# Optimization experiments

Hardware: AMD Instinct MI355X
Metric: run time of the kernel (lower is better)

Reference implementation:

```python
import jax, jax.numpy as jnp
import numpy as np

B, L, D, H = 2, 2048, 2048, 16
DH = D // H
SCALE = 1.0 / float(np.sqrt(DH))


def setup_inputs() -> dict:
    key = jax.random.key(0)
    ks = jax.random.split(key, 5)
    std = 1.0 / float(np.sqrt(D))
    return {
        "x": jax.random.normal(ks[0], (B, L, D), dtype=jnp.float32),
        "W_q": jax.random.normal(ks[1], (D, D), dtype=jnp.float32) * std,
        "W_k": jax.random.normal(ks[2], (D, D), dtype=jnp.float32) * std,
        "W_v": jax.random.normal(ks[3], (D, D), dtype=jnp.float32) * std,
        "W_o": jax.random.normal(ks[4], (D, D), dtype=jnp.float32) * std,
    }


def _split_heads(t):
    # (B, L, D) -> (B, H, L, DH)
    b, l, _ = t.shape
    return t.reshape(b, l, H, DH).transpose(0, 2, 1, 3)


def reference(x, W_q, W_k, W_v, W_o):
    # nn.Linear(bias=False): y = x @ W.T
    q = _split_heads(x @ W_q.T)  # (B,H,L,DH)
    k = _split_heads(x @ W_k.T)
    v = _split_heads(x @ W_v.T)
    scores = jnp.einsum("bhqd,bhkd->bhqk", q, k) * SCALE  # (B,H,L,L)
    causal = jnp.arange(L)[:, None] >= jnp.arange(L)[None, :]  # True = keep
    scores = jnp.where(causal[None, None], scores, -jnp.inf)
    attn = jax.nn.softmax(scores, axis=-1)
    y = jnp.einsum("bhqk,bhkd->bhqd", attn, v)  # (B,H,L,DH)
    y = y.transpose(0, 2, 1, 3).reshape(B, L, D)  # merge heads
    return y @ W_o.T
```

## Files before the change

### kernel.cpp

```cpp
#include <hip/hip_runtime.h>
#include <hip/hip_bf16.h>
#include <stdint.h>

typedef unsigned short u16;
typedef __bf16 bf16x8 __attribute__((ext_vector_type(8)));
typedef float f32x4 __attribute__((ext_vector_type(4)));

#define SEQ    2048
#define DMODEL 2048
#define NHEAD  16
#define DHEAD  128
#define QSCALE (0.088388347648318447f * 1.4426950408889634f)

__device__ __forceinline__ u16 f2bf(float f){
  uint32_t u = __float_as_uint(f);
  u += 0x7FFFu + ((u >> 16) & 1u);
  return (u16)(u >> 16);
}

__device__ __forceinline__ void gload_lds16(const u16* g, u16* l){
  __builtin_amdgcn_global_load_lds((const __attribute__((address_space(1))) void*)g,
                                   (__attribute__((address_space(3))) void*)l,
                                   16, 0, 0);
}

__global__ __launch_bounds__(256) void cvt_bf16(const float* __restrict__ src,
                                                u16* __restrict__ dst, int n4){
  int i = blockIdx.x * 256 + threadIdx.x;
  if (i < n4){
    float4 v = reinterpret_cast<const float4*>(src)[i];
    ushort4 o;
    o.x = f2bf(v.x); o.y = f2bf(v.y); o.z = f2bf(v.z); o.w = f2bf(v.w);
    reinterpret_cast<ushort4*>(dst)[i] = o;
  }
}

__global__ __launch_bounds__(256) void cvt_w4(const float* __restrict__ Wq,
    const float* __restrict__ Wk, const float* __restrict__ Wv,
    const float* __restrict__ Wo, u16* __restrict__ dst){
  const int z = blockIdx.y;
  const float* s = (z==0) ? Wq : (z==1) ? Wk : (z==2) ? Wv : Wo;
  int i = blockIdx.x * 256 + threadIdx.x;
  float4 v = reinterpret_cast<const float4*>(s)[i];
  ushort4 o;
  o.x = f2bf(v.x); o.y = f2bf(v.y); o.z = f2bf(v.z); o.w = f2bf(v.w);
  reinterpret_cast<ushort4*>(dst + (size_t)z*4194304)[i] = o;
}

__device__ __forceinline__ void stageA(const u16* __restrict__ G, int grow0, int kt,
                                       int half, u16* lds, int w, int lane){
  #pragma unroll
  for (int j = 0; j < 2; ++j){
    int q   = w*2 + j;
    int r0  = ((q & 8) << 4) + half*64 + (q & 7)*8;
    int row = r0 + (lane >> 3);
    int sc  = (lane & 7) ^ (row & 7);
    gload_lds16(G + (size_t)(grow0 + row)*DMODEL + kt*64 + sc*8, lds + r0*64);
  }
}
__device__ __forceinline__ void stageB(const u16* __restrict__ G, int grow0, int kt,
                                       int half, u16* lds, int w, int lane){
  #pragma unroll
  for (int j = 0; j < 2; ++j){
    int q   = w*2 + j;
    int r0  = ((q >> 2) << 6) + half*32 + (q & 3)*8;
    int row = r0 + (lane >> 3);
    int sc  = (lane & 7) ^ (row & 7);
    gload_lds16(G + (size_t)(grow0 + row)*DMODEL + kt*64 + sc*8, lds + r0*64);
  }
}

__device__ __forceinline__ bf16x8 ldsf(const u16* lds, int row, int c){
  return *reinterpret_cast<const bf16x8*>(lds + row*64 + (((c ^ (row & 7)) & 7) << 3));
}

template<int MH>
__device__ __forceinline__ void load_a(bf16x8 (&a)[4][2], const u16* LA,
                                       int wr, int ln, int g){
  #pragma unroll
  for (int m = 0; m < 4; ++m){
    int row = wr*128 + MH*64 + m*16 + ln;
    a[m][0] = ldsf(LA, row, g);
    a[m][1] = ldsf(LA, row, 4 + g);
  }
}
template<int NH>
__device__ __forceinline__ void load_b(bf16x8 (&b)[2][2], const u16* LB,
                                       int wc, int ln, int g){
  #pragma unroll
  for (int n = 0; n < 2; ++n){
    int row = wc*64 + NH*32 + n*16 + ln;
    b[n][0] = ldsf(LB, row, g);
    b[n][1] = ldsf(LB, row, 4 + g);
  }
}

template<int MH, int NH>
__device__ __forceinline__ void mfma_quad(f32x4 (&acc)[8][4], bf16x8 (&a)[4][2],
                                          bf16x8 (&b)[2][2]){
  __builtin_amdgcn_s_setprio(1);
  #pragma unroll
  for (int m = 0; m < 4; ++m)
    #pragma unroll
    for (int n = 0; n < 2; ++n){
      acc[MH*4+m][NH*2+n] = __builtin_amdgcn_mfma_f32_16x16x32_bf16(
          a[m][0], b[n][0], acc[MH*4+m][NH*2+n], 0, 0, 0);
      acc[MH*4+m][NH*2+n] = __builtin_amdgcn_mfma_f32_16x16x32_bf16(
          a[m][1], b[n][1], acc[MH*4+m][NH*2+n], 0, 0, 0);
    }
  __builtin_amdgcn_s_setprio(0);
}

__device__ __forceinline__ void phase_pre(){
  __builtin_amdgcn_s_barrier();
  asm volatile("s_waitcnt lgkmcnt(0)" ::: "memory");
  __builtin_amdgcn_sched_barrier(0);
}

__device__ __forceinline__ void gemm8_core(const u16* __restrict__ A,
    const u16* __restrict__ W, int bm, int bnl,
    u16 (*ldsA)[256*64], u16 (*ldsB)[256*64], f32x4 (&acc)[8][4],
    int w, int lane, int wr, int wc, int g, int ln){
  const f32x4 z4 = {0.f,0.f,0.f,0.f};
  #pragma unroll
  for (int i = 0; i < 8; ++i)
    #pragma unroll
    for (int j = 0; j < 4; ++j) acc[i][j] = z4;

  stageA(A, bm, 0, 0, ldsA[0], w, lane);
  stageB(W, bnl, 0, 1, ldsB[0], w, lane);
  stageA(A, bm, 0, 1, ldsA[0], w, lane);
  stageB(W, bnl, 0, 0, ldsB[0], w, lane);
  stageA(A, bm, 1, 0, ldsA[1], w, lane);
  stageB(W, bnl, 1, 1, ldsB[1], w, lane);
  asm volatile("s_waitcnt vmcnt(4)" ::: "memory");
  __builtin_amdgcn_s_barrier();

  bf16x8 a[4][2], b[2][2];
  const int NT = DMODEL/64;
  for (int t = 0; t < NT; ++t){
    const int cur = t & 1;
    const u16* LA = ldsA[cur];
    const u16* LB = ldsB[cur];
    load_a<0>(a, LA, wr, ln, g);
    load_b<0>(b, LB, wc, ln, g);
    if (t+1 < NT) stageA(A, bm, t+1, 1, ldsA[cur^1], w, lane);
    phase_pre();
    mfma_quad<0,0>(acc, a, b);
    __builtin_amdgcn_s_barrier();
    load_b<1>(b, LB, wc, ln, g);
    if (t+1 < NT) stageB(W, bnl, t+1, 0, ldsB[cur^1], w, lane);
    phase_pre();
    mfma_quad<0,1>(acc, a, b);
    __builtin_amdgcn_s_barrier();
    load_a<1>(a, LA, wr, ln, g);
    if (t+2 < NT) stageA(A, bm, t+2, 0, ldsA[cur], w, lane);
    phase_pre();
    mfma_quad<1,1>(acc, a, b);
    __builtin_amdgcn_s_barrier();
    load_b<0>(b, LB, wc, ln, g);
    if (t+2 < NT) stageB(W, bnl, t+2, 1, ldsB[cur], w, lane);
    if (t < NT-2) { asm volatile("s_waitcnt vmcnt(4)" ::: "memory"); }
    else          { asm volatile("s_waitcnt vmcnt(0)" ::: "memory"); }
    phase_pre();
    mfma_quad<1,0>(acc, a, b);
    __builtin_amdgcn_s_barrier();
  }
}

__global__ __launch_bounds__(512, 2) void gemm_qkv8(const u16* __restrict__ A,
    const u16* __restrict__ Wall, u16* __restrict__ Q, u16* __restrict__ Kb,
    u16* __restrict__ Vt){
  __shared__ __align__(16) u16 ldsA[2][256*64];
  __shared__ __align__(16) u16 ldsB[2][256*64];
  const int tid = threadIdx.x, w = tid >> 6, lane = tid & 63;
  const int g = lane >> 4, ln = lane & 15;
  const int wr = w >> 2, wc = w & 3;
  const int bid = blockIdx.x;
  const int swz = (bid & 7)*48 + (bid >> 3);
  const int nt = swz >> 4, mt = swz & 15;
  const int bm = mt*256, z = nt >> 3, bnl = (nt & 7) << 8;
  const u16* W = Wall + ((size_t)z << 22);
  f32x4 acc[8][4];
  gemm8_core(A, W, bm, bnl, ldsA, ldsB, acc, w, lane, wr, wc, g, ln);

  if (z < 2){
    u16* C = (z == 0) ? Q : Kb;
    const float sc = (z == 0) ? QSCALE : 1.0f;
    #pragma unroll
    for (int mf = 0; mf < 8; ++mf)
      #pragma unroll
      for (int nf = 0; nf < 4; ++nf){
        int col = bnl + wc*64 + nf*16 + ln;
        #pragma unroll
        for (int i = 0; i < 4; ++i){
          int row = bm + wr*128 + mf*16 + g*4 + i;
          C[(size_t)row*DMODEL + col] = f2bf(acc[mf][nf][i] * sc);
        }
      }
  } else {
    #pragma unroll
    for (int mf = 0; mf < 8; ++mf)
      #pragma unroll
      for (int nf = 0; nf < 4; ++nf){
        int col  = bnl + wc*64 + nf*16 + ln;
        int row0 = bm + wr*128 + mf*16 + g*4;
        int bb   = row0 >> 11, lt = row0 & (SEQ-1);
        ushort4 pk;
        pk.x = f2bf(acc[mf][nf][0]); pk.y = f2bf(acc[mf][nf][1]);
        pk.z = f2bf(acc[mf][nf][2]); pk.w = f2bf(acc[mf][nf][3]);
        *reinterpret_cast<ushort4*>(Vt + (size_t)(bb*DMODEL + col)*SEQ + lt) = pk;
      }
  }
}

__global__ __launch_bounds__(512, 2) void gemm_out8(const u16* __restrict__ A,
    const u16* __restrict__ Wo, float* __restrict__ C){
  __shared__ __align__(16) u16 ldsA[2][256*64];
  __shared__ __align__(16) u16 ldsB[2][256*64];
  const int tid = threadIdx.x, w = tid >> 6, lane = tid & 63;
  const int g = lane >> 4, ln = lane & 15;
  const int wr = w >> 2, wc = w & 3;
  const int bid = blockIdx.x;
  const int swz = (bid & 7)*16 + (bid >> 3);
  const int nt = swz >> 4, mt = swz & 15;
  const int bm = mt*256, bnl = nt << 8;
  f32x4 acc[8][4];
  gemm8_core(A, Wo, bm, bnl, ldsA, ldsB, acc, w, lane, wr, wc, g, ln);
  #pragma unroll
  for (int mf = 0; mf < 8; ++mf)
    #pragma unroll
    for (int nf = 0; nf < 4; ++nf){
      int col = bnl + wc*64 + nf*16 + ln;
      #pragma unroll
      for (int i = 0; i < 4; ++i){
        int row = bm + wr*128 + mf*16 + g*4 + i;
        C[(size_t)row*DMODEL + col] = acc[mf][nf][i];
      }
    }
}


__device__ __forceinline__ void attn_stageK(const u16* __restrict__ Kb,
    u16* Kt, int b, int h, int kb, int w, int lane){
  #pragma unroll
  for (int is = 0; is < 4; ++is){
    int o = w*4096 + is*1024 + lane*16;
    int row = o >> 8;
    int sc  = ((o >> 4) & 15) ^ (row & 7);
    gload_lds16(Kb + (size_t)(b*SEQ + kb + row)*DMODEL + h*DHEAD + sc*8,
                Kt + w*2048 + is*512);
  }
}
__device__ __forceinline__ void attn_stageV(const u16* __restrict__ Vtb,
    u16* Vt, int bh, int kb, int w, int lane){
  #pragma unroll
  for (int is = 0; is < 4; ++is){
    int o = w*4096 + is*1024 + lane*16;
    int row = o >> 7;
    int sc  = ((o >> 4) & 7) ^ (row & 7);
    gload_lds16(Vtb + (size_t)(bh*DHEAD + row)*SEQ + kb + sc*8,
                Vt + w*2048 + is*512);
  }
}

template<bool MASKED>
__device__ __forceinline__ void attn_qkt_sm(const u16* Kt, u16* Pw,
    const bf16x8 (&qf)[2][4], f32x4 (&yacc)[2][8],
    float (&mrun)[2], float (&lrun)[2],
    int kb, int qg0, int g, int ln){
  #pragma unroll
  for (int qc = 0; qc < 2; ++qc){
    f32x4 st[4];
    __builtin_amdgcn_s_setprio(1);
    #pragma unroll
    for (int kt = 0; kt < 4; ++kt){
      f32x4 accs = {0.f,0.f,0.f,0.f};
      #pragma unroll
      for (int c = 0; c < 4; ++c){
        int row = kt*16 + ln;
        int ch  = (c*4 + g) ^ (row & 7);
        bf16x8 kf = *reinterpret_cast<const bf16x8*>(Kt + row*128 + ch*8);
        accs = __builtin_amdgcn_mfma_f32_16x16x32_bf16(kf, qf[qc][c], accs, 0, 0, 0);
      }
      st[kt] = accs;
    }
    __builtin_amdgcn_s_setprio(0);

    const int qg = qg0 + qc*16;
    float p[16];
    float tmax = -1e30f;
    #pragma unroll
    for (int kt = 0; kt < 4; ++kt)
      #pragma unroll
      for (int i = 0; i < 4; ++i){
        float s = st[kt][i];
        if (MASKED && (kb + kt*16 + g*4 + i) > qg) s = -1e30f;
        p[kt*4+i] = s;
        tmax = fmaxf(tmax, s);
      }
    tmax = fmaxf(tmax, __shfl_xor(tmax, 16));
    tmax = fmaxf(tmax, __shfl_xor(tmax, 32));

    if (!__all(tmax - mrun[qc] <= 11.5f)){
      float mn = fmaxf(mrun[qc], tmax);
      float fr = __builtin_amdgcn_exp2f(mrun[qc] - mn);
      lrun[qc] *= fr;
      float fi[4];
      #pragma unroll
      for (int i = 0; i < 4; ++i) fi[i] = __shfl(fr, g*4 + i);
      #pragma unroll
      for (int dt = 0; dt < 8; ++dt)
        #pragma unroll
        for (int i = 0; i < 4; ++i) yacc[qc][dt][i] *= fi[i];
      mrun[qc] = mn;
    }
    float psum = 0.f;
    #pragma unroll
    for (int j = 0; j < 16; ++j){
      p[j] = __builtin_amdgcn_exp2f(p[j] - mrun[qc]);
      psum += p[j];
    }
    psum += __shfl_xor(psum, 16);
    psum += __shfl_xor(psum, 32);
    lrun[qc] += psum;

    char* pb = reinterpret_cast<char*>(Pw + qc*1024);
    #pragma unroll
    for (int kt = 0; kt < 4; ++kt)
      #pragma unroll
      for (int pr = 0; pr < 2; ++pr){
        uint32_t pk = (uint32_t)f2bf(p[kt*4 + 2*pr]) |
                      ((uint32_t)f2bf(p[kt*4 + 2*pr + 1]) << 16);
        int byte = (kt*16 + g*4 + 2*pr)*2;
        int ch   = (byte >> 4) ^ (ln & 7);
        int addr = ln*128 + (ch << 4) + (byte & 15);
        *reinterpret_cast<uint32_t*>(pb + addr) = pk;
      }
  }
}

__device__ __forceinline__ void attn_pv(const u16* Vt, const u16* Pw,
                                        f32x4 (&yacc)[2][8], int g, int ln){
  __builtin_amdgcn_s_setprio(1);
  #pragma unroll
  for (int kc = 0; kc < 2; ++kc){
    int chp = (kc*4 + g) ^ (ln & 7);
    bf16x8 pf0 = *reinterpret_cast<const bf16x8*>(Pw +        ln*64 + chp*8);
    bf16x8 pf1 = *reinterpret_cast<const bf16x8*>(Pw + 1024 + ln*64 + chp*8);
    #pragma unroll
    for (int dt = 0; dt < 8; ++dt){
      int row = dt*16 + ln;
      int chv = (kc*4 + g) ^ (row & 7);
      bf16x8 vf = *reinterpret_cast<const bf16x8*>(Vt + row*64 + chv*8);
      yacc[0][dt] = __builtin_amdgcn_mfma_f32_16x16x32_bf16(pf0, vf, yacc[0][dt], 0, 0, 0);
      yacc[1][dt] = __builtin_amdgcn_mfma_f32_16x16x32_bf16(pf1, vf, yacc[1][dt], 0, 0, 0);
    }
  }
  __builtin_amdgcn_s_setprio(0);
}

__global__ __launch_bounds__(256, 2) void attn_fwd(const u16* __restrict__ Qb,
    const u16* __restrict__ Kb, const u16* __restrict__ Vtb, u16* __restrict__ Yb){
  __shared__ __align__(16) u16 Kt[2][64*128];
  __shared__ __align__(16) u16 Vt[2][128*64];
  __shared__ __align__(16) u16 Pl[4][2048];
  const int tid = threadIdx.x, w = tid >> 6, lane = tid & 63;
  const int g = lane >> 4, ln = lane & 15;
  const int bh = blockIdx.y;
  const int b = bh >> 4, h = bh & 15;
  const int qb = (bh < 16) ? blockIdx.x : (15 - blockIdx.x);
  const int qw = qb*128 + w*32;
  const int qg0 = qw + ln;
  const int NT = 2*qb + 2;

  bf16x8 qf[2][4];
  #pragma unroll
  for (int qc = 0; qc < 2; ++qc){
    const u16* qp = Qb + (size_t)(b*SEQ + qw + qc*16 + ln)*DMODEL + h*DHEAD + g*8;
    #pragma unroll
    for (int c = 0; c < 4; ++c) qf[qc][c] = *reinterpret_cast<const bf16x8*>(qp + c*32);
  }
  float mrun[2] = {-1e30f, -1e30f}, lrun[2] = {0.f, 0.f};
  f32x4 yacc[2][8];
  {
    const f32x4 z4 = {0.f,0.f,0.f,0.f};
    #pragma unroll
    for (int qc = 0; qc < 2; ++qc)
      #pragma unroll
      for (int dt = 0; dt < 8; ++dt) yacc[qc][dt] = z4;
  }
  u16* Pw = &Pl[w][0];

  attn_stageK(Kb, &Kt[0][0], b, h, 0, w, lane);
  attn_stageV(Vtb, &Vt[0][0], bh, 0, w, lane);
  asm volatile("s_waitcnt vmcnt(0)" ::: "memory");
  __builtin_amdgcn_s_barrier();

  int cur = 0;
  for (int t = 0; t < NT; ++t){
    const int kb = t*64;
    if (t+1 < NT){
      attn_stageK(Kb, &Kt[cur^1][0], b, h, kb + 64, w, lane);
      attn_stageV(Vtb, &Vt[cur^1][0], bh, kb + 64, w, lane);
    }
    if (t < NT-2)
      attn_qkt_sm<false>(&Kt[cur][0], Pw, qf, yacc, mrun, lrun, kb, qg0, g, ln);
    else
      attn_qkt_sm<true >(&Kt[cur][0], Pw, qf, yacc, mrun, lrun, kb, qg0, g, ln);
    attn_pv(&Vt[cur][0], Pw, yacc, g, ln);
    asm volatile("s_waitcnt vmcnt(0) lgkmcnt(0)" ::: "memory");
    __builtin_amdgcn_s_barrier();
    cur ^= 1;
  }

  #pragma unroll
  for (int qc = 0; qc < 2; ++qc){
    float inv[4];
    #pragma unroll
    for (int i = 0; i < 4; ++i){
      float li = __shfl(lrun[qc], g*4 + i);
      inv[i] = __builtin_amdgcn_rcpf(li);
    }
    #pragma unroll
    for (int dt = 0; dt < 8; ++dt)
      #pragma unroll
      for (int i = 0; i < 4; ++i){
        Yb[(size_t)(b*SEQ + qw + qc*16 + g*4 + i)*DMODEL + h*DHEAD + dt*16 + ln] =
            f2bf(yacc[qc][dt][i] * inv[i]);
      }
  }
}

extern "C" void kernel_launch(void* const* d_in, const int* in_sizes, int n_in,
                              void* d_out, int out_size, void* d_ws, size_t ws_size,
                              hipStream_t stream) {
  const float* x  = (const float*)d_in[0];
  const float* Wq = (const float*)d_in[1];
  const float* Wk = (const float*)d_in[2];
  const float* Wv = (const float*)d_in[3];
  const float* Wo = (const float*)d_in[4];
  float* out = (float*)d_out;

  char* ws = (char*)d_ws;
  u16* xb  = (u16*)(ws +          0);
  u16* Wqb = (u16*)(ws + 16777216);
  u16* Wob = (u16*)(ws + 41943040);
  u16* Qb  = (u16*)(ws + 50331648);
  u16* Kb  = (u16*)(ws + 67108864);
  u16* Vtb = (u16*)(ws + 83886080);
  u16* Yb  = (u16*)(ws + 100663296);

  cvt_bf16<<<dim3(8192), 256, 0, stream>>>(x, xb, 2097152);
  cvt_w4<<<dim3(4096, 4), 256, 0, stream>>>(Wq, Wk, Wv, Wo, Wqb);

  gemm_qkv8<<<dim3(384), 512, 0, stream>>>(xb, Wqb, Qb, Kb, Vtb);

  attn_fwd<<<dim3(16, 32), 256, 0, stream>>>(Qb, Kb, Vtb, Yb);

  gemm_out8<<<dim3(128), 512, 0, stream>>>(Yb, Wob, out);
}
```

Measured before the change: 298.1 us.

## Halve GEMM block M-tile to 128 rows and restage the double-buffered pipeline

Both projection GEMMs now use 128x256 block tiles instead of 256x256, doubling the grid to 768 QKV blocks and 256 output-projection blocks. The aim is to fill more of the CUs, especially in the output projection, which previously launched only 128 blocks. The LDS staging is rewritten as uniform 64-row units: A and the first B quarter are prefetched one k-step ahead, and the remaining B rows two steps ahead. The k-loop now has two MFMA phases instead of four. In exchange, per-block arithmetic intensity drops, B tiles get more re-reads, and the QKV grid exceeds one full wave at two blocks per CU.

Measured after the change: 311.1 us. 1.04x slower.

```diff
diff --git a/kernel.cpp b/kernel.cpp
--- a/kernel.cpp
+++ b/kernel.cpp
@@ -47,27 +47,13 @@
   reinterpret_cast<ushort4*>(dst + (size_t)z*4194304)[i] = o;
 }
 
-__device__ __forceinline__ void stageA(const u16* __restrict__ G, int grow0, int kt,
-                                       int half, u16* lds, int w, int lane){
-  #pragma unroll
-  for (int j = 0; j < 2; ++j){
-    int q   = w*2 + j;
-    int r0  = ((q & 8) << 4) + half*64 + (q & 7)*8;
-    int row = r0 + (lane >> 3);
-    int sc  = (lane & 7) ^ (row & 7);
-    gload_lds16(G + (size_t)(grow0 + row)*DMODEL + kt*64 + sc*8, lds + r0*64);
-  }
-}
-__device__ __forceinline__ void stageB(const u16* __restrict__ G, int grow0, int kt,
-                                       int half, u16* lds, int w, int lane){
-  #pragma unroll
-  for (int j = 0; j < 2; ++j){
-    int q   = w*2 + j;
-    int r0  = ((q >> 2) << 6) + half*32 + (q & 3)*8;
-    int row = r0 + (lane >> 3);
-    int sc  = (lane & 7) ^ (row & 7);
-    gload_lds16(G + (size_t)(grow0 + row)*DMODEL + kt*64 + sc*8, lds + r0*64);
-  }
+
+__device__ __forceinline__ void stage_unit(const u16* __restrict__ G, int grow0,
+    int kt, int row0, u16* lds, int w, int lane){
+  int row = row0 + w*8 + (lane >> 3);
+  int sc  = (lane & 7) ^ (row & 7);
+  gload_lds16(G + (size_t)(grow0 + row)*DMODEL + kt*64 + sc*8,
+              lds + (row0 + w*8)*64);
 }
 
 __device__ __forceinline__ bf16x8 ldsf(const u16* lds, int row, int c){
@@ -75,38 +61,37 @@
 }
 
 template<int MH>
-__device__ __forceinline__ void load_a(bf16x8 (&a)[4][2], const u16* LA,
-                                       int wr, int ln, int g){
-  #pragma unroll
-  for (int m = 0; m < 4; ++m){
-    int row = wr*128 + MH*64 + m*16 + ln;
+__device__ __forceinline__ void load_a2(bf16x8 (&a)[2][2], const u16* LA,
+                                        int wr, int ln, int g){
+  #pragma unroll
+  for (int m = 0; m < 2; ++m){
+    int row = wr*64 + MH*32 + m*16 + ln;
     a[m][0] = ldsf(LA, row, g);
     a[m][1] = ldsf(LA, row, 4 + g);
   }
 }
-template<int NH>
-__device__ __forceinline__ void load_b(bf16x8 (&b)[2][2], const u16* LB,
-                                       int wc, int ln, int g){
-  #pragma unroll
-  for (int n = 0; n < 2; ++n){
-    int row = wc*64 + NH*32 + n*16 + ln;
+__device__ __forceinline__ void load_b4(bf16x8 (&b)[4][2], const u16* LB,
+                                        int wc, int ln, int g){
+  #pragma unroll
+  for (int n = 0; n < 4; ++n){
+    int row = wc*64 + n*16 + ln;
     b[n][0] = ldsf(LB, row, g);
     b[n][1] = ldsf(LB, row, 4 + g);
   }
 }
 
-template<int MH, int NH>
-__device__ __forceinline__ void mfma_quad(f32x4 (&acc)[8][4], bf16x8 (&a)[4][2],
-                                          bf16x8 (&b)[2][2]){
+template<int MH>
+__device__ __forceinline__ void mfma_half(f32x4 (&acc)[4][4], bf16x8 (&a)[2][2],
+                                          bf16x8 (&b)[4][2]){
   __builtin_amdgcn_s_setprio(1);
   #pragma unroll
-  for (int m = 0; m < 4; ++m)
-    #pragma unroll
-    for (int n = 0; n < 2; ++n){
-      acc[MH*4+m][NH*2+n] = __builtin_amdgcn_mfma_f32_16x16x32_bf16(
-          a[m][0], b[n][0], acc[MH*4+m][NH*2+n], 0, 0, 0);
-      acc[MH*4+m][NH*2+n] = __builtin_amdgcn_mfma_f32_16x16x32_bf16(
-          a[m][1], b[n][1], acc[MH*4+m][NH*2+n], 0, 0, 0);
+  for (int m = 0; m < 2; ++m)
+    #pragma unroll
+    for (int n = 0; n < 4; ++n){
+      acc[MH*2+m][n] = __builtin_amdgcn_mfma_f32_16x16x32_bf16(
+          a[m][0], b[n][0], acc[MH*2+m][n], 0, 0, 0);
+      acc[MH*2+m][n] = __builtin_amdgcn_mfma_f32_16x16x32_bf16(
+          a[m][1], b[n][1], acc[MH*2+m][n], 0, 0, 0);
     }
   __builtin_amdgcn_s_setprio(0);
 }
@@ -117,94 +102,96 @@
   __builtin_amdgcn_sched_barrier(0);
 }
 
-__device__ __forceinline__ void gemm8_core(const u16* __restrict__ A,
+__device__ __forceinline__ void gemm2_core(const u16* __restrict__ A,
     const u16* __restrict__ W, int bm, int bnl,
-    u16 (*ldsA)[256*64], u16 (*ldsB)[256*64], f32x4 (&acc)[8][4],
+    u16 (*ldsA)[128*64], u16 (*ldsB)[256*64], f32x4 (&acc)[4][4],
     int w, int lane, int wr, int wc, int g, int ln){
   const f32x4 z4 = {0.f,0.f,0.f,0.f};
   #pragma unroll
-  for (int i = 0; i < 8; ++i)
+  for (int i = 0; i < 4; ++i)
     #pragma unroll
     for (int j = 0; j < 4; ++j) acc[i][j] = z4;
 
-  stageA(A, bm, 0, 0, ldsA[0], w, lane);
-  stageB(W, bnl, 0, 1, ldsB[0], w, lane);
-  stageA(A, bm, 0, 1, ldsA[0], w, lane);
-  stageB(W, bnl, 0, 0, ldsB[0], w, lane);
-  stageA(A, bm, 1, 0, ldsA[1], w, lane);
-  stageB(W, bnl, 1, 1, ldsB[1], w, lane);
-  asm volatile("s_waitcnt vmcnt(4)" ::: "memory");
+  stage_unit(A, bm, 0, 0,   ldsA[0], w, lane);
+  stage_unit(A, bm, 0, 64,  ldsA[0], w, lane);
+  stage_unit(W, bnl, 0, 0,   ldsB[0], w, lane);
+  stage_unit(W, bnl, 0, 64,  ldsB[0], w, lane);
+  stage_unit(W, bnl, 0, 128, ldsB[0], w, lane);
+  stage_unit(W, bnl, 0, 192, ldsB[0], w, lane);
+  stage_unit(W, bnl, 1, 64,  ldsB[1], w, lane);
+  stage_unit(W, bnl, 1, 128, ldsB[1], w, lane);
+  stage_unit(W, bnl, 1, 192, ldsB[1], w, lane);
+  asm volatile("s_waitcnt vmcnt(3)" ::: "memory");
   __builtin_amdgcn_s_barrier();
 
-  bf16x8 a[4][2], b[2][2];
+  bf16x8 a[2][2], b[4][2];
   const int NT = DMODEL/64;
   for (int t = 0; t < NT; ++t){
     const int cur = t & 1;
     const u16* LA = ldsA[cur];
     const u16* LB = ldsB[cur];
-    load_a<0>(a, LA, wr, ln, g);
-    load_b<0>(b, LB, wc, ln, g);
-    if (t+1 < NT) stageA(A, bm, t+1, 1, ldsA[cur^1], w, lane);
+    load_a2<0>(a, LA, wr, ln, g);
+    load_b4(b, LB, wc, ln, g);
+    if (t+1 < NT){
+      stage_unit(A, bm, t+1, 0,  ldsA[cur^1], w, lane);
+      stage_unit(A, bm, t+1, 64, ldsA[cur^1], w, lane);
+      stage_unit(W, bnl, t+1, 0, ldsB[cur^1], w, lane);
+    }
     phase_pre();
-    mfma_quad<0,0>(acc, a, b);
+    mfma_half<0>(acc, a, b);
     __builtin_amdgcn_s_barrier();
-    load_b<1>(b, LB, wc, ln, g);
-    if (t+1 < NT) stageB(W, bnl, t+1, 0, ldsB[cur^1], w, lane);
+    load_a2<1>(a, LA, wr, ln, g);
+    if (t+2 < NT){
+      stage_unit(W, bnl, t+2, 64,  ldsB[cur], w, lane);
+      stage_unit(W, bnl, t+2, 128, ldsB[cur], w, lane);
+      stage_unit(W, bnl, t+2, 192, ldsB[cur], w, lane);
+      asm volatile("s_waitcnt vmcnt(3)" ::: "memory");
+    } else {
+      asm volatile("s_waitcnt vmcnt(0)" ::: "memory");
+    }
     phase_pre();
-    mfma_quad<0,1>(acc, a, b);
+    mfma_half<1>(acc, a, b);
     __builtin_amdgcn_s_barrier();
-    load_a<1>(a, LA, wr, ln, g);
-    if (t+2 < NT) stageA(A, bm, t+2, 0, ldsA[cur], w, lane);
-    phase_pre();
-    mfma_quad<1,1>(acc, a, b);
-    __builtin_amdgcn_s_barrier();
-    load_b<0>(b, LB, wc, ln, g);
-    if (t+2 < NT) stageB(W, bnl, t+2, 1, ldsB[cur], w, lane);
-    if (t < NT-2) { asm volatile("s_waitcnt vmcnt(4)" ::: "memory"); }
-    else          { asm volatile("s_waitcnt vmcnt(0)" ::: "memory"); }
-    phase_pre();
-    mfma_quad<1,0>(acc, a, b);
-    __builtin_amdgcn_s_barrier();
-  }
-}
-
-__global__ __launch_bounds__(512, 2) void gemm_qkv8(const u16* __restrict__ A,
+  }
+}
+
+__global__ __launch_bounds__(512, 2) void gemm_qkv2(const u16* __restrict__ A,
     const u16* __restrict__ Wall, u16* __restrict__ Q, u16* __restrict__ Kb,
     u16* __restrict__ Vt){
-  __shared__ __align__(16) u16 ldsA[2][256*64];
+  __shared__ __align__(16) u16 ldsA[2][128*64];
   __shared__ __align__(16) u16 ldsB[2][256*64];
   const int tid = threadIdx.x, w = tid >> 6, lane = tid & 63;
   const int g = lane >> 4, ln = lane & 15;
   const int wr = w >> 2, wc = w & 3;
   const int bid = blockIdx.x;
-  const int swz = (bid & 7)*48 + (bid >> 3);
-  const int nt = swz >> 4, mt = swz & 15;
-  const int bm = mt*256, z = nt >> 3, bnl = (nt & 7) << 8;
+  const int swz = (bid & 7)*96 + (bid >> 3);
+  const int nt = swz >> 5, mt = swz & 31;
+  const int bm = mt*128, z = nt >> 3, bnl = (nt & 7) << 8;
   const u16* W = Wall + ((size_t)z << 22);
-  f32x4 acc[8][4];
-  gemm8_core(A, W, bm, bnl, ldsA, ldsB, acc, w, lane, wr, wc, g, ln);
+  f32x4 acc[4][4];
+  gemm2_core(A, W, bm, bnl, ldsA, ldsB, acc, w, lane, wr, wc, g, ln);
 
   if (z < 2){
     u16* C = (z == 0) ? Q : Kb;
     const float sc = (z == 0) ? QSCALE : 1.0f;
     #pragma unroll
-    for (int mf = 0; mf < 8; ++mf)
+    for (int mf = 0; mf < 4; ++mf)
       #pragma unroll
       for (int nf = 0; nf < 4; ++nf){
         int col = bnl + wc*64 + nf*16 + ln;
         #pragma unroll
         for (int i = 0; i < 4; ++i){
-          int row = bm + wr*128 + mf*16 + g*4 + i;
+          int row = bm + wr*64 + mf*16 + g*4 + i;
           C[(size_t)row*DMODEL + col] = f2bf(acc[mf][nf][i] * sc);
         }
       }
   } else {
     #pragma unroll
-    for (int mf = 0; mf < 8; ++mf)
+    for (int mf = 0; mf < 4; ++mf)
       #pragma unroll
       for (int nf = 0; nf < 4; ++nf){
         int col  = bnl + wc*64 + nf*16 + ln;
-        int row0 = bm + wr*128 + mf*16 + g*4;
+        int row0 = bm + wr*64 + mf*16 + g*4;
         int bb   = row0 >> 11, lt = row0 & (SEQ-1);
         ushort4 pk;
         pk.x = f2bf(acc[mf][nf][0]); pk.y = f2bf(acc[mf][nf][1]);
@@ -214,32 +201,31 @@
   }
 }
 
-__global__ __launch_bounds__(512, 2) void gemm_out8(const u16* __restrict__ A,
+__global__ __launch_bounds__(512, 2) void gemm_out2(const u16* __restrict__ A,
     const u16* __restrict__ Wo, float* __restrict__ C){
-  __shared__ __align__(16) u16 ldsA[2][256*64];
+  __shared__ __align__(16) u16 ldsA[2][128*64];
   __shared__ __align__(16) u16 ldsB[2][256*64];
   const int tid = threadIdx.x, w = tid >> 6, lane = tid & 63;
   const int g = lane >> 4, ln = lane & 15;
   const int wr = w >> 2, wc = w & 3;
   const int bid = blockIdx.x;
-  const int swz = (bid & 7)*16 + (bid >> 3);
-  const int nt = swz >> 4, mt = swz & 15;
-  const int bm = mt*256, bnl = nt << 8;
-  f32x4 acc[8][4];
-  gemm8_core(A, Wo, bm, bnl, ldsA, ldsB, acc, w, lane, wr, wc, g, ln);
-  #pragma unroll
-  for (int mf = 0; mf < 8; ++mf)
+  const int swz = (bid & 7)*32 + (bid >> 3);
+  const int nt = swz >> 5, mt = swz & 31;
+  const int bm = mt*128, bnl = nt << 8;
+  f32x4 acc[4][4];
+  gemm2_core(A, Wo, bm, bnl, ldsA, ldsB, acc, w, lane, wr, wc, g, ln);
+  #pragma unroll
+  for (int mf = 0; mf < 4; ++mf)
     #pragma unroll
     for (int nf = 0; nf < 4; ++nf){
       int col = bnl + wc*64 + nf*16 + ln;
       #pragma unroll
       for (int i = 0; i < 4; ++i){
-        int row = bm + wr*128 + mf*16 + g*4 + i;
+        int row = bm + wr*64 + mf*16 + g*4 + i;
         C[(size_t)row*DMODEL + col] = acc[mf][nf][i];
       }
     }
 }
-
 
 __device__ __forceinline__ void attn_stageK(const u16* __restrict__ Kb,
     u16* Kt, int b, int h, int kb, int w, int lane){
@@ -454,9 +440,9 @@
   cvt_bf16<<<dim3(8192), 256, 0, stream>>>(x, xb, 2097152);
   cvt_w4<<<dim3(4096, 4), 256, 0, stream>>>(Wq, Wk, Wv, Wo, Wqb);
 
-  gemm_qkv8<<<dim3(384), 512, 0, stream>>>(xb, Wqb, Qb, Kb, Vtb);
+  gemm_qkv2<<<dim3(768), 512, 0, stream>>>(xb, Wqb, Qb, Kb, Vtb);
 
   attn_fwd<<<dim3(16, 32), 256, 0, stream>>>(Qb, Kb, Vtb, Yb);
 
-  gemm_out8<<<dim3(128), 512, 0, stream>>>(Yb, Wob, out);
-}
+  gemm_out2<<<dim3(256), 512, 0, stream>>>(Yb, Wob, out);
+}
```

## Use 256x128 tiles for output projection to fill all CUs

Applied to the files above, without the earlier changes.

The output projection GEMM changes from 256x256 tiles (128 blocks) to 256x128 tiles (256 blocks), which roughly matches the CU count on MI355X and reduces idle hardware. It adds a dedicated pipelined main loop that double-buffers half-sized B tiles and interleaves MFMA octets with async global-to-LDS staging. In exchange, each block does less arithmetic per byte loaded, so A tiles are re-read twice as often from L2.

Result: faster. 290.6 us (-2.5%).

```diff
diff --git a/kernel.cpp b/kernel.cpp
--- a/kernel.cpp
+++ b/kernel.cpp
@@ -214,24 +214,98 @@
   }
 }
 
-__global__ __launch_bounds__(512, 2) void gemm_out8(const u16* __restrict__ A,
+__device__ __forceinline__ void stageB2(const u16* __restrict__ G, int grow0,
+    int kt, int half, u16* lds, int w, int lane){
+  int r0  = half*64 + (w & 7)*8;
+  int row = r0 + (lane >> 3);
+  int sc  = (lane & 7) ^ (row & 7);
+  gload_lds16(G + (size_t)(grow0 + row)*DMODEL + kt*64 + sc*8, lds + r0*64);
+}
+
+template<int NH>
+__device__ __forceinline__ void load_b2(bf16x8 (&b)[2], const u16* LB,
+                                        int wc, int ln, int g){
+  int row = NH*64 + wc*16 + ln;
+  b[0] = ldsf(LB, row, g);
+  b[1] = ldsf(LB, row, 4 + g);
+}
+
+template<int MH, int NH>
+__device__ __forceinline__ void mfma_oct(f32x4 (&acc)[8][2], bf16x8 (&a)[4][2],
+                                         bf16x8 (&b)[2]){
+  __builtin_amdgcn_s_setprio(1);
+  #pragma unroll
+  for (int m = 0; m < 4; ++m){
+    acc[MH*4+m][NH] = __builtin_amdgcn_mfma_f32_16x16x32_bf16(
+        a[m][0], b[0], acc[MH*4+m][NH], 0, 0, 0);
+    acc[MH*4+m][NH] = __builtin_amdgcn_mfma_f32_16x16x32_bf16(
+        a[m][1], b[1], acc[MH*4+m][NH], 0, 0, 0);
+  }
+  __builtin_amdgcn_s_setprio(0);
+}
+
+__global__ __launch_bounds__(512, 2) void gemm_out2(const u16* __restrict__ A,
     const u16* __restrict__ Wo, float* __restrict__ C){
   __shared__ __align__(16) u16 ldsA[2][256*64];
-  __shared__ __align__(16) u16 ldsB[2][256*64];
+  __shared__ __align__(16) u16 ldsB[2][128*64];
   const int tid = threadIdx.x, w = tid >> 6, lane = tid & 63;
   const int g = lane >> 4, ln = lane & 15;
   const int wr = w >> 2, wc = w & 3;
   const int bid = blockIdx.x;
-  const int swz = (bid & 7)*16 + (bid >> 3);
+  const int swz = (bid & 7)*32 + (bid >> 3);
   const int nt = swz >> 4, mt = swz & 15;
-  const int bm = mt*256, bnl = nt << 8;
-  f32x4 acc[8][4];
-  gemm8_core(A, Wo, bm, bnl, ldsA, ldsB, acc, w, lane, wr, wc, g, ln);
+  const int bm = mt*256, bnl = nt << 7;
+  f32x4 acc[8][2];
+  {
+    const f32x4 z4 = {0.f,0.f,0.f,0.f};
+    #pragma unroll
+    for (int i = 0; i < 8; ++i){ acc[i][0] = z4; acc[i][1] = z4; }
+  }
+  stageA (A,  bm,  0, 0, ldsA[0], w, lane);
+  stageA (A,  bm,  0, 1, ldsA[0], w, lane);
+  stageB2(Wo, bnl, 0, 0, ldsB[0], w, lane);
+  stageB2(Wo, bnl, 0, 1, ldsB[0], w, lane);
+  stageA (A,  bm,  1, 0, ldsA[1], w, lane);
+  stageB2(Wo, bnl, 1, 1, ldsB[1], w, lane);
+  asm volatile("s_waitcnt vmcnt(3)" ::: "memory");
+  __builtin_amdgcn_s_barrier();
+
+  bf16x8 a[4][2], b0[2], b1[2];
+  const int NT = DMODEL/64;
+  for (int t = 0; t < NT; ++t){
+    const int cur = t & 1;
+    const u16* LA = ldsA[cur];
+    const u16* LB = ldsB[cur];
+    load_a<0>(a, LA, wr, ln, g);
+    load_b2<0>(b0, LB, wc, ln, g);
+    if (t+1 < NT) stageA(A, bm, t+1, 1, ldsA[cur^1], w, lane);
+    phase_pre();
+    mfma_oct<0,0>(acc, a, b0);
+    __builtin_amdgcn_s_barrier();
+    load_b2<1>(b1, LB, wc, ln, g);
+    if (t+1 < NT) stageB2(Wo, bnl, t+1, 0, ldsB[cur^1], w, lane);
+    phase_pre();
+    mfma_oct<0,1>(acc, a, b1);
+    __builtin_amdgcn_s_barrier();
+    load_a<1>(a, LA, wr, ln, g);
+    if (t+2 < NT) stageA(A, bm, t+2, 0, ldsA[cur], w, lane);
+    phase_pre();
+    mfma_oct<1,1>(acc, a, b1);
+    __builtin_amdgcn_s_barrier();
+    load_b2<0>(b0, LB, wc, ln, g);
+    if (t+2 < NT) stageB2(Wo, bnl, t+2, 1, ldsB[cur], w, lane);
+    if (t < NT-2) { asm volatile("s_waitcnt vmcnt(3)" ::: "memory"); }
+    else          { asm volatile("s_waitcnt vmcnt(0)" ::: "memory"); }
+    phase_pre();
+    mfma_oct<1,0>(acc, a, b0);
+    __builtin_amdgcn_s_barrier();
+  }
+
   #pragma unroll
   for (int mf = 0; mf < 8; ++mf)
     #pragma unroll
-    for (int nf = 0; nf < 4; ++nf){
-      int col = bnl + wc*64 + nf*16 + ln;
+    for (int nf = 0; nf < 2; ++nf){
+      int col = bnl + nf*64 + wc*16 + ln;
       #pragma unroll
       for (int i = 0; i < 4; ++i){
         int row = bm + wr*128 + mf*16 + g*4 + i;
@@ -239,7 +313,6 @@
       }
     }
 }
-
 
 __device__ __forceinline__ void attn_stageK(const u16* __restrict__ Kb,
     u16* Kt, int b, int h, int kb, int w, int lane){
@@ -458,5 +531,5 @@
 
   attn_fwd<<<dim3(16, 32), 256, 0, stream>>>(Qb, Kb, Vtb, Yb);
 
-  gemm_out8<<<dim3(128), 512, 0, stream>>>(Yb, Wob, out);
-}
+  gemm_out2<<<dim3(256), 512, 0, stream>>>(Yb, Wob, out);
+}
```
